# Performance work log

Measured on AMD Instinct MI355X. Metric: run time of the kernel, lower is better.

Reference implementation:

```python
import jax, jax.numpy as jnp
import numpy as np

N, E = 32768, 524288
NIN = NOUT = 64
EIN = 32
H, C = 4, 64
HC = H * C


def seg_softmax(logits, seg, num):
    m = jax.ops.segment_max(logits, seg, num_segments=num)
    m = jnp.where(jnp.isfinite(m), m, 0.0)
    ex = jnp.exp(logits - m[seg])
    s = jax.ops.segment_sum(ex, seg, num_segments=num)
    return ex / (s[seg] + 1e-16)


def setup_inputs() -> dict:
    key = jax.random.key(0)
    ks = iter(jax.random.split(key, 48))
    rn = lambda shape, s=0.05: jax.random.normal(next(ks), shape, jnp.float32) * s
    z = lambda shape: jnp.zeros(shape, jnp.float32)
    d = dict(
        x=rn((N, NIN), 1.0),
        edge_attr=rn((E, EIN), 1.0),
        # GINEConv 1: nn = mlp1 (64 -> 64 -> 64), edge lin (32 -> 64), eps
        eps1=z(()), w1a=rn((NIN, 64)), b1a=z((64,)), w1b=rn((64, NOUT)), b1b=z((NOUT,)),
        we1=rn((EIN, NIN)), be1=z((NIN,)),
        # GINEConv 2: nn = mlp2 (64 -> 32 -> 64), edge lin (32 -> 64), eps
        eps2=z(()), w2a=rn((NOUT, 32)), b2a=z((32,)), w2b=rn((32, NOUT)), b2b=z((NOUT,)),
        we2=rn((EIN, NOUT)), be2=z((NOUT,)),
        # TransformerConv(64, 64, heads=4, edge_dim=32)
        wq=rn((NOUT, HC)), bq=z((HC,)), wk=rn((NOUT, HC)), bk=z((HC,)),
        wv=rn((NOUT, HC)), bv=z((HC,)), we3=rn((EIN, HC)),
        wskip=rn((NOUT, HC)), bskip=z((HC,)),
        # GATv2Conv(256, 64, heads=1, edge_dim=32)
        wl=rn((HC, NOUT)), bl=z((NOUT,)), wr=rn((HC, NOUT)), br=z((NOUT,)),
        we4=rn((EIN, NOUT)), att=rn((NOUT,)), bias4=z((NOUT,)),
    )
    d['edge_index'] = jax.random.randint(next(ks), (2, E), 0, N, dtype=jnp.int64)
    return d


def _forward(x, edge_attr, eps1, w1a, b1a, w1b, b1b, we1, be1,
             eps2, w2a, b2a, w2b, b2b, we2, be2,
             wq, bq, wk, bk, wv, bv, we3, wskip, bskip,
             wl, bl, wr, br, we4, att, bias4, edge_index):
    src, dst = edge_index[0], edge_index[1]
    n = x.shape[0]

    # --- GINEConv 1: nn((1+eps)*x + sum_j relu(x_j + lin_e(e_ij))) ---
    e1 = edge_attr @ we1 + be1                                  # (E, NIN)
    agg = jax.ops.segment_sum(jax.nn.relu(x[src] + e1), dst, num_segments=n)
    h = (1.0 + eps1) * x + agg
    x = jax.nn.relu(h @ w1a + b1a) @ w1b + b1b                  # (N, NOUT)

    # --- GINEConv 2 ---
    e2 = edge_attr @ we2 + be2
    agg = jax.ops.segment_sum(jax.nn.relu(x[src] + e2), dst, num_segments=n)
    h = (1.0 + eps2) * x + agg
    x = jax.nn.relu(h @ w2a + b2a) @ w2b + b2b                  # (N, NOUT)

    # --- TransformerConv (heads=4, concat, root skip) ---
    q = (x @ wq + bq).reshape(n, H, C)
    k = (x @ wk + bk).reshape(n, H, C)
    v = (x @ wv + bv).reshape(n, H, C)
    e3 = (edge_attr @ we3).reshape(-1, H, C)
    kj = k[src] + e3
    alpha = jnp.einsum('ehc,ehc->eh', q[dst], kj) / jnp.sqrt(jnp.float32(C))
    alpha = seg_softmax(alpha, dst, n)                          # (E, H)
    msg = (v[src] + e3) * alpha[:, :, None]                     # (E, H, C)
    out = jax.ops.segment_sum(msg, dst, num_segments=n).reshape(n, HC)
    x = out + x @ wskip + bskip                                 # (N, 256)

    # --- GATv2Conv (heads=1) ---
    xl = x @ wl + bl                                            # (N, NOUT)
    xr = x @ wr + br
    e4 = edge_attr @ we4
    hmsg = jax.nn.leaky_relu(xl[src] + xr[dst] + e4, 0.2)       # (E, NOUT)
    logit = hmsg @ att                                          # (E,)
    a = seg_softmax(logit, dst, n)
    x = jax.ops.segment_sum(xl[src] * a[:, None], dst, num_segments=n) + bias4
    return x


def reference(x, edge_attr, eps1, w1a, b1a, w1b, b1b, we1, be1,
              eps2, w2a, b2a, w2b, b2b, we2, be2,
              wq, bq, wk, bk, wv, bv, we3, wskip, bskip,
              wl, bl, wr, br, we4, att, bias4, edge_index):
    return _forward(x, edge_attr, eps1, w1a, b1a, w1b, b1b, we1, be1,
                    eps2, w2a, b2a, w2b, b2b, we2, be2,
                    wq, bq, wk, bk, wv, bv, we3, wskip, bskip,
                    wl, bl, wr, br, we4, att, bias4, edge_index)
```

## Files before the change

kernel.cpp:

```cpp
#include <hip/hip_runtime.h>
#include <math.h>


typedef __attribute__((ext_vector_type(2))) _Float16 half2v;
typedef __attribute__((ext_vector_type(4))) _Float16 half4v;
typedef __attribute__((ext_vector_type(8))) _Float16 half8v;
typedef __attribute__((ext_vector_type(4))) float float4v;

__global__ void k_detect(const unsigned int* __restrict__ w, int* __restrict__ flag)
{
    __shared__ int any;
    if (threadIdx.x == 0) any = 0;
    __syncthreads();
    int found = 0;
    for (int i = threadIdx.x; i < 2048; i += 256)
        if (w[2 * i + 1] != 0u) found = 1;
    if (found) atomicOr(&any, 1);
    __syncthreads();
    if (threadIdx.x == 0) flag[0] = any ? 0 : 1;
}

__global__ void k_cvt(const void* __restrict__ eidx, const int* __restrict__ flag,
                      int* __restrict__ out, int* __restrict__ counts, int E)
{
    int i = blockIdx.x * blockDim.x + threadIdx.x;
    if (i >= 2 * E) return;
    int v = flag[0] ? (int)((const long long*)eidx)[i] : ((const int*)eidx)[i];
    out[i] = v;
    if (i >= E) atomicAdd(&counts[v], 1);
}

__global__ void k_scan(const int* __restrict__ counts, int* __restrict__ offs,
                       int* __restrict__ cursor, int N)
{
    __shared__ int part[1024];
    int t = threadIdx.x;
    int base = t * 32;
    int loc[32];
    int s = 0;
#pragma unroll
    for (int i = 0; i < 32; i++) { loc[i] = counts[base + i]; s += loc[i]; }
    part[t] = s;
    __syncthreads();
    for (int off = 1; off < 1024; off <<= 1) {
        int v = (t >= off) ? part[t - off] : 0;
        __syncthreads();
        part[t] += v;
        __syncthreads();
    }
    int run = part[t] - s;
#pragma unroll
    for (int i = 0; i < 32; i++) {
        offs[base + i] = run;
        cursor[base + i] = run;
        run += loc[i];
    }
    if (t == 1023) offs[N] = run;
}

__global__ void k_scatter(const int* __restrict__ dst, const int* __restrict__ srcA,
                          int* __restrict__ cursor, int* __restrict__ perm,
                          int* __restrict__ sperm, int E)
{
    int i = blockIdx.x * blockDim.x + threadIdx.x;
    if (i >= E) return;
    int d = dst[i];
    int p = atomicAdd(&cursor[d], 1);
    perm[p] = i;
    sperm[p] = srcA[i];
}

template<int WEAP, int DUAL>
__global__ __launch_bounds__(256) void k_emm2(
    const float* __restrict__ ea, const int* __restrict__ perm,
    const _Float16* __restrict__ WtA, const float* __restrict__ beA,
    _Float16* __restrict__ epA,
    const _Float16* __restrict__ WtB, const float* __restrict__ beB,
    _Float16* __restrict__ epB,
    _Float16* __restrict__ eap)
{
    __shared__ _Float16 st[4][16][72];
    int t = threadIdx.x;
    int wid = t >> 6, l = t & 63;
    int jb = (blockIdx.x * 4 + wid) * 16;
    int cr = l & 15, kg = l >> 4;
    int e = perm[jb + cr];
    const float* ar = ea + (size_t)e * 32 + kg * 8;
    float4 f0 = *(const float4*)ar;
    float4 f1 = *(const float4*)(ar + 4);
    half8v a;
    a[0] = (_Float16)f0.x; a[1] = (_Float16)f0.y;
    a[2] = (_Float16)f0.z; a[3] = (_Float16)f0.w;
    a[4] = (_Float16)f1.x; a[5] = (_Float16)f1.y;
    a[6] = (_Float16)f1.z; a[7] = (_Float16)f1.w;
    if (WEAP)
        *(half8v*)&eap[(size_t)(jb + cr) * 32 + kg * 8] = a;
    _Float16 (*S)[72] = st[wid];
    int rr = l >> 2, cs = (l & 3) * 16;
#pragma unroll
    for (int c = 0; c < 4; c++) {
        half8v b = *(const half8v*)&WtA[(size_t)(c * 16 + cr) * 32 + kg * 8];
        float4v d = __builtin_amdgcn_mfma_f32_16x16x32_f16(a, b, (float4v){0.f,0.f,0.f,0.f}, 0, 0, 0);
        int col = c * 16 + cr;
        float bv = beA ? beA[col] : 0.f;
#pragma unroll
        for (int r = 0; r < 4; r++)
            S[kg * 4 + r][col] = (_Float16)(d[r] + bv);
    }
    {
        half8v v0 = *(const half8v*)&S[rr][cs];
        half8v v1 = *(const half8v*)&S[rr][cs + 8];
        *(half8v*)&epA[(size_t)(jb + rr) * 64 + cs] = v0;
        *(half8v*)&epA[(size_t)(jb + rr) * 64 + cs + 8] = v1;
    }
    if (DUAL) {
#pragma unroll
        for (int c = 0; c < 4; c++) {
            half8v b = *(const half8v*)&WtB[(size_t)(c * 16 + cr) * 32 + kg * 8];
            float4v d = __builtin_amdgcn_mfma_f32_16x16x32_f16(a, b, (float4v){0.f,0.f,0.f,0.f}, 0, 0, 0);
            int col = c * 16 + cr;
            float bv = beB ? beB[col] : 0.f;
#pragma unroll
            for (int r = 0; r < 4; r++)
                S[kg * 4 + r][col] = (_Float16)(d[r] + bv);
        }
        half8v v0 = *(const half8v*)&S[rr][cs];
        half8v v1 = *(const half8v*)&S[rr][cs + 8];
        *(half8v*)&epB[(size_t)(jb + rr) * 64 + cs] = v0;
        *(half8v*)&epB[(size_t)(jb + rr) * 64 + cs + 8] = v1;
    }
}

__global__ __launch_bounds__(256) void k_emm(
    const _Float16* __restrict__ eap,
    const _Float16* __restrict__ WtA, const float* __restrict__ beA,
    _Float16* __restrict__ epA)
{
    __shared__ _Float16 st[4][16][72];
    int t = threadIdx.x;
    int wid = t >> 6, l = t & 63;
    int jb = (blockIdx.x * 4 + wid) * 16;
    int cr = l & 15, kg = l >> 4;
    half8v a = *(const half8v*)&eap[(size_t)(jb + cr) * 32 + kg * 8];
    _Float16 (*S)[72] = st[wid];
#pragma unroll
    for (int c = 0; c < 4; c++) {
        half8v b = *(const half8v*)&WtA[(size_t)(c * 16 + cr) * 32 + kg * 8];
        float4v d = __builtin_amdgcn_mfma_f32_16x16x32_f16(a, b, (float4v){0.f,0.f,0.f,0.f}, 0, 0, 0);
        int col = c * 16 + cr;
        float bv = beA ? beA[col] : 0.f;
#pragma unroll
        for (int r = 0; r < 4; r++)
            S[kg * 4 + r][col] = (_Float16)(d[r] + bv);
    }
    int rr = l >> 2, cs = (l & 3) * 16;
    half8v v0 = *(const half8v*)&S[rr][cs];
    half8v v1 = *(const half8v*)&S[rr][cs + 8];
    *(half8v*)&epA[(size_t)(jb + rr) * 64 + cs] = v0;
    *(half8v*)&epA[(size_t)(jb + rr) * 64 + cs + 8] = v1;
}

__global__ __launch_bounds__(256) void k_prep(
    const float* __restrict__ x, int NX,
    const float* __restrict__ wq, const float* __restrict__ wk,
    const float* __restrict__ wv, const float* __restrict__ wskip,
    const float* __restrict__ wl, const float* __restrict__ wr,
    const float* __restrict__ w1a, const float* __restrict__ w1b,
    const float* __restrict__ w2a, const float* __restrict__ w2b,
    const float* __restrict__ we3, const float* __restrict__ bq,
    const float* __restrict__ we1, const float* __restrict__ we2,
    const float* __restrict__ we4,
    _Float16* __restrict__ xh,
    _Float16* __restrict__ Wts, _Float16* __restrict__ Gt,
    _Float16* __restrict__ Wtl, _Float16* __restrict__ Wtr,
    _Float16* __restrict__ Wt1a, _Float16* __restrict__ Wt1b,
    _Float16* __restrict__ Wt2a, _Float16* __restrict__ Wt2b,
    _Float16* __restrict__ Mt, float* __restrict__ cst,
    _Float16* __restrict__ Wt1e, _Float16* __restrict__ Wt2e,
    _Float16* __restrict__ Wt4e, float* __restrict__ zt,
    _Float16* __restrict__ Bt3)
{
    int g = blockIdx.x * 256 + threadIdx.x;
    if (g < 16384) {
        int c = g >> 6, k = g & 63;
        Wts[g] = (_Float16)wskip[(size_t)k * 256 + c];
    } else if (g < 32768) {
        int q = g - 16384, col = q >> 6, d = q & 63;
        int h = col >> 6, c = col & 63;
        float s = 0.f;
        for (int mq = 0; mq < 64; mq++)
            s = fmaf(wq[(size_t)d * 256 + h * 64 + mq],
                     wk[(size_t)c * 256 + h * 64 + mq], s);
        Gt[q] = (_Float16)(0.125f * s);
    } else if (g < 49152) {
        int q = g - 32768, c = q >> 8, k = q & 255;
        Wtl[q] = (_Float16)wl[(size_t)k * 64 + c];
        Wtr[q] = (_Float16)wr[(size_t)k * 64 + c];
    } else if (g < 53248) {
        int q = g - 49152, m = q >> 6, k = q & 63;
        Wt1a[q] = (_Float16)w1a[(size_t)k * 64 + m];
        Wt1b[q] = (_Float16)w1b[(size_t)k * 64 + m];
    } else if (g < 55296) {
        int q = g - 53248, m = q >> 6, k = q & 63;
        Wt2a[q] = (_Float16)w2a[(size_t)k * 32 + m];
    } else if (g < 57344) {
        int q = g - 55296, c = q >> 5, k = q & 31;
        Wt2b[q] = (_Float16)w2b[(size_t)k * 64 + c];
    } else if (g < 65536) {
        int q = g - 57344, m = q >> 6, d = q & 63;
        int h = m >> 5, kk = m & 31;
        float s = 0.f;
        for (int c = 0; c < 64; c++)
            s = fmaf(wq[(size_t)d * 256 + h * 64 + c],
                     we3[(size_t)kk * 256 + h * 64 + c], s);
        Mt[q] = (_Float16)(0.125f * s);
    } else if (g < 65664) {
        int m = g - 65536, h = m >> 5, kk = m & 31;
        float s = 0.f;
        for (int c = 0; c < 64; c++)
            s = fmaf(bq[h * 64 + c], we3[(size_t)kk * 256 + h * 64 + c], s);
        cst[m] = 0.125f * s;
    } else if (g < 67712) {
        int q = g - 65664, c = q >> 5, k = q & 31;
        Wt1e[q] = (_Float16)we1[(size_t)k * 64 + c];
    } else if (g < 69760) {
        int q = g - 67712, c = q >> 5, k = q & 31;
        Wt2e[q] = (_Float16)we2[(size_t)k * 64 + c];
    } else if (g < 71808) {
        int q = g - 69760, c = q >> 5, k = q & 31;
        Wt4e[q] = (_Float16)we4[(size_t)k * 64 + c];
    } else if (g < 72064) {
        int q = g - 71808, h = q >> 6, c = q & 63;
        float s = 0.f;
        for (int mq = 0; mq < 64; mq++)
            s = fmaf(wk[(size_t)c * 256 + h * 64 + mq], bq[h * 64 + mq], s);
        zt[q] = 0.125f * s;
    } else if (g < 96640) {
        int q = g - 72064;
        int hc = q / 96, k = q - hc * 96;
        int h = hc >> 6, col = hc & 63;
        float v = (k < 64) ? wv[(size_t)k * 256 + h * 64 + col]
                           : we3[(size_t)(k - 64) * 256 + h * 64 + col];
        Bt3[q] = (_Float16)v;
    }
    for (int i = g; i < NX; i += 512 * 256)
        xh[i] = (_Float16)x[i];
}

template<int MID>
__global__ __launch_bounds__(256) void k_mlp(
    const _Float16* __restrict__ A,
    const _Float16* __restrict__ Wt1, const float* __restrict__ b1,
    const _Float16* __restrict__ Wt2, const float* __restrict__ b2,
    _Float16* __restrict__ out)
{
    __shared__ _Float16 As[64][72];
    __shared__ _Float16 Ws1[MID][72];
    __shared__ _Float16 Ws2[64][MID + 8];
    __shared__ _Float16 mids[64][MID + 8];
    int t = threadIdx.x;
    int n0 = blockIdx.x * 64;
    for (int f = t; f < 512; f += 256) {
        int r = f >> 3, seg = f & 7;
        *(uint4*)&As[r][seg * 8] = *(const uint4*)&A[(size_t)(n0 + r) * 64 + seg * 8];
    }
    for (int f = t; f < MID * 8; f += 256) {
        int r = f >> 3, seg = f & 7;
        *(uint4*)&Ws1[r][seg * 8] = *(const uint4*)&Wt1[(size_t)r * 64 + seg * 8];
    }
    constexpr int CH = MID / 8;
    for (int f = t; f < 64 * CH; f += 256) {
        int r = f / CH, seg = f % CH;
        *(uint4*)&Ws2[r][seg * 8] = *(const uint4*)&Wt2[(size_t)r * MID + seg * 8];
    }
    __syncthreads();
    int w = t >> 6, l = t & 63;
    int arow = w * 16 + (l & 15);
    int kg = (l >> 4) * 8;
    int colg = l & 15;
    int orow = w * 16 + (l >> 4) * 4;
    half8v a0 = *(const half8v*)&As[arow][kg];
    half8v a1 = *(const half8v*)&As[arow][32 + kg];
    constexpr int NCT1 = MID / 16;
#pragma unroll
    for (int ct = 0; ct < NCT1; ct++) {
        half8v b0 = *(const half8v*)&Ws1[ct * 16 + colg][kg];
        half8v b1v = *(const half8v*)&Ws1[ct * 16 + colg][32 + kg];
        float4v acc = {0.f, 0.f, 0.f, 0.f};
        acc = __builtin_amdgcn_mfma_f32_16x16x32_f16(a0, b0, acc, 0, 0, 0);
        acc = __builtin_amdgcn_mfma_f32_16x16x32_f16(a1, b1v, acc, 0, 0, 0);
        int col = ct * 16 + colg;
        float bb = b1[col];
#pragma unroll
        for (int r = 0; r < 4; r++)
            mids[orow + r][col] = (_Float16)fmaxf(acc[r] + bb, 0.f);
    }
    __syncthreads();
    half8v m0 = *(const half8v*)&mids[arow][kg];
#pragma unroll
    for (int ct = 0; ct < 4; ct++) {
        half8v b0 = *(const half8v*)&Ws2[ct * 16 + colg][kg];
        float4v acc = {0.f, 0.f, 0.f, 0.f};
        acc = __builtin_amdgcn_mfma_f32_16x16x32_f16(m0, b0, acc, 0, 0, 0);
        if (MID == 64) {
            half8v m1 = *(const half8v*)&mids[arow][32 + kg];
            half8v b1v = *(const half8v*)&Ws2[ct * 16 + colg][32 + kg];
            acc = __builtin_amdgcn_mfma_f32_16x16x32_f16(m1, b1v, acc, 0, 0, 0);
        }
        int col = ct * 16 + colg;
        float bb = b2[col];
#pragma unroll
        for (int r = 0; r < 4; r++)
            out[(size_t)(n0 + orow + r) * 64 + col] = (_Float16)(acc[r] + bb);
    }
}

__global__ __launch_bounds__(256) void k_gemm4m(
    const _Float16* __restrict__ A,
    const _Float16* __restrict__ Gt,
    const _Float16* __restrict__ Wts, const float* __restrict__ bs,
    const _Float16* __restrict__ Mt,  const float* __restrict__ cst,
    _Float16* __restrict__ Yb, _Float16* __restrict__ skiph,
    _Float16* __restrict__ qtp)
{
    __shared__ _Float16 As[64][72];
    __shared__ _Float16 Ws[128][72];
    int t = threadIdx.x;
    int n0 = blockIdx.x * 64;
    int y = blockIdx.y;
    for (int f = t; f < 512; f += 256) {
        int r = f >> 3, seg = f & 7;
        *(uint4*)&As[r][seg * 8] = *(const uint4*)&A[(size_t)(n0 + r) * 64 + seg * 8];
    }
    if (y < 8) {
        int j0 = (y & 3) * 64;
        const _Float16* Wt = (y < 4) ? Gt : Wts;
        for (int f = t; f < 512; f += 256) {
            int c = f >> 3, seg = f & 7;
            *(uint4*)&Ws[c][seg * 8] = *(const uint4*)&Wt[(size_t)(j0 + c) * 64 + seg * 8];
        }
    } else {
        for (int f = t; f < 1024; f += 256) {
            int c = f >> 3, seg = f & 7;
            *(uint4*)&Ws[c][seg * 8] = *(const uint4*)&Mt[(size_t)c * 64 + seg * 8];
        }
    }
    __syncthreads();
    int w = t >> 6, l = t & 63;
    int arow = w * 16 + (l & 15);
    int kg = (l >> 4) * 8;
    int colg = l & 15;
    int orow = w * 16 + (l >> 4) * 4;
    half8v a0 = *(const half8v*)&As[arow][kg];
    half8v a1 = *(const half8v*)&As[arow][32 + kg];
    if (y < 8) {
        int j0 = (y & 3) * 64;
        _Float16* O = (y < 4) ? Yb : skiph;
#pragma unroll
        for (int ct = 0; ct < 4; ct++) {
            half8v b0 = *(const half8v*)&Ws[ct * 16 + colg][kg];
            half8v b1 = *(const half8v*)&Ws[ct * 16 + colg][32 + kg];
            float4v a = {0.f, 0.f, 0.f, 0.f};
            a = __builtin_amdgcn_mfma_f32_16x16x32_f16(a0, b0, a, 0, 0, 0);
            a = __builtin_amdgcn_mfma_f32_16x16x32_f16(a1, b1, a, 0, 0, 0);
            int col = j0 + ct * 16 + colg;
            float bb = (y < 4) ? 0.f : bs[col];
#pragma unroll
            for (int r = 0; r < 4; r++)
                O[(size_t)(n0 + orow + r) * 256 + col] = (_Float16)(a[r] + bb);
        }
    } else {
#pragma unroll
        for (int ct = 0; ct < 8; ct++) {
            half8v b0 = *(const half8v*)&Ws[ct * 16 + colg][kg];
            half8v b1 = *(const half8v*)&Ws[ct * 16 + colg][32 + kg];
            float4v a = {0.f, 0.f, 0.f, 0.f};
            a = __builtin_amdgcn_mfma_f32_16x16x32_f16(a0, b0, a, 0, 0, 0);
            a = __builtin_amdgcn_mfma_f32_16x16x32_f16(a1, b1, a, 0, 0, 0);
            int col = ct * 16 + colg;
            float bb = cst[col];
#pragma unroll
            for (int r = 0; r < 4; r++)
                qtp[(size_t)(n0 + orow + r) * 128 + col] = (_Float16)(a[r] + bb);
        }
    }
}

__global__ __launch_bounds__(256) void k_gine2(
    const _Float16* __restrict__ xin, const _Float16* __restrict__ ep,
    const float* __restrict__ epsp,
    const int* __restrict__ offs, const int* __restrict__ sperm,
    _Float16* __restrict__ hout)
{
    int t = threadIdx.x;
    int wid  = __builtin_amdgcn_readfirstlane(t >> 6);
    int n    = blockIdx.x * 4 + wid;
    int lane = t & 63;
    int g = lane >> 4, li = lane & 15, c0 = li * 4;
    int j0 = __builtin_amdgcn_readfirstlane(offs[n]);
    int j1 = __builtin_amdgcn_readfirstlane(offs[n + 1]);
    float4 acc = {0.f, 0.f, 0.f, 0.f};
    for (int jq = j0; jq < j1; jq += 4) {
        int j = jq + g;
        int jc = (j < j1) ? j : (j1 - 1);
        int s = sperm[jc];
        half4v ev = *(const half4v*)&ep[(size_t)jc * 64 + c0];
        half4v xv = *(const half4v*)&xin[(size_t)s * 64 + c0];
        if (j < j1) {
            acc.x += fmaxf((float)xv[0] + (float)ev[0], 0.f);
            acc.y += fmaxf((float)xv[1] + (float)ev[1], 0.f);
            acc.z += fmaxf((float)xv[2] + (float)ev[2], 0.f);
            acc.w += fmaxf((float)xv[3] + (float)ev[3], 0.f);
        }
    }
    acc.x += __shfl_xor(acc.x, 16); acc.x += __shfl_xor(acc.x, 32);
    acc.y += __shfl_xor(acc.y, 16); acc.y += __shfl_xor(acc.y, 32);
    acc.z += __shfl_xor(acc.z, 16); acc.z += __shfl_xor(acc.z, 32);
    acc.w += __shfl_xor(acc.w, 16); acc.w += __shfl_xor(acc.w, 32);
    if (g == 0) {
        float eps1 = 1.f + epsp[0];
        half4v xn = *(const half4v*)&xin[(size_t)n * 64 + c0];
        half4v o;
        o[0] = (_Float16)(eps1 * (float)xn[0] + acc.x);
        o[1] = (_Float16)(eps1 * (float)xn[1] + acc.y);
        o[2] = (_Float16)(eps1 * (float)xn[2] + acc.z);
        o[3] = (_Float16)(eps1 * (float)xn[3] + acc.w);
        *(half4v*)&hout[(size_t)n * 64 + c0] = o;
    }
}

template<int USE_EAP>
__global__ __launch_bounds__(256) void k_tconv5(
    const _Float16* __restrict__ Yb, const _Float16* __restrict__ qtp,
    const float* __restrict__ zt, const _Float16* __restrict__ x2h,
    const _Float16* __restrict__ eap, const float* __restrict__ ea,
    const int* __restrict__ perm, const int* __restrict__ offs,
    const int* __restrict__ sperm,
    _Float16* __restrict__ xaccb, _Float16* __restrict__ wab,
    float* __restrict__ lb)
{
    int t = threadIdx.x;
    int wid = __builtin_amdgcn_readfirstlane(t >> 6);
    int n = blockIdx.x * 4 + wid;
    int lane = t & 63;
    int h = lane >> 4, c = lane & 15;
    float yb0, yb1, yb2, yb3;
    {
        half4v Y4 = *(const half4v*)&Yb[(size_t)n * 256 + h * 64 + c * 4];
        float4 z4 = *(const float4*)&zt[h * 64 + c * 4];
        yb0 = (float)Y4[0] + z4.x; yb1 = (float)Y4[1] + z4.y;
        yb2 = (float)Y4[2] + z4.z; yb3 = (float)Y4[3] + z4.w;
    }
    half2v qt2 = *(const half2v*)&qtp[(size_t)n * 128 + h * 32 + c * 2];
    float qt0 = (float)qt2[0], qt1 = (float)qt2[1];
    int j0 = __builtin_amdgcn_readfirstlane(offs[n]);
    int j1 = __builtin_amdgcn_readfirstlane(offs[n + 1]);
    float l = 0.f;
    float xa0 = 0.f, xa1 = 0.f, xa2 = 0.f, xa3 = 0.f;
    float wa0 = 0.f, wa1 = 0.f;
    int j = j0;
    for (; j + 1 < j1; j += 2) {
        int s0 = __builtin_amdgcn_readfirstlane(sperm[j]);
        int s1 = __builtin_amdgcn_readfirstlane(sperm[j + 1]);
        half4v xA = *(const half4v*)&x2h[(size_t)s0 * 64 + c * 4];
        half4v xB = *(const half4v*)&x2h[(size_t)s1 * 64 + c * 4];
        float eA0, eA1, eB0, eB1;
        if (USE_EAP) {
            half2v vA = *(const half2v*)&eap[(size_t)j * 32 + c * 2];
            half2v vB = *(const half2v*)&eap[(size_t)(j + 1) * 32 + c * 2];
            eA0 = (float)vA[0]; eA1 = (float)vA[1];
            eB0 = (float)vB[0]; eB1 = (float)vB[1];
        } else {
            int e0 = __builtin_amdgcn_readfirstlane(perm[j]);
            int e1 = __builtin_amdgcn_readfirstlane(perm[j + 1]);
            float2 fA = *(const float2*)&ea[(size_t)e0 * 32 + c * 2];
            float2 fB = *(const float2*)&ea[(size_t)e1 * 32 + c * 2];
            eA0 = fA.x; eA1 = fA.y; eB0 = fB.x; eB1 = fB.y;
        }
        float xA0 = (float)xA[0], xA1f = (float)xA[1];
        float xA2 = (float)xA[2], xA3 = (float)xA[3];
        float xB0 = (float)xB[0], xB1f = (float)xB[1];
        float xB2 = (float)xB[2], xB3 = (float)xB[3];
        float p0 = yb0 * xA0 + yb1 * xA1f + yb2 * xA2 + yb3 * xA3
                 + qt0 * eA0 + qt1 * eA1;
        float p1 = yb0 * xB0 + yb1 * xB1f + yb2 * xB2 + yb3 * xB3
                 + qt0 * eB0 + qt1 * eB1;
        p0 += __shfl_xor(p0, 1); p1 += __shfl_xor(p1, 1);
        p0 += __shfl_xor(p0, 2); p1 += __shfl_xor(p1, 2);
        p0 += __shfl_xor(p0, 4); p1 += __shfl_xor(p1, 4);
        p0 += __shfl_xor(p0, 8); p1 += __shfl_xor(p1, 8);
        float w0 = __expf(p0), w1 = __expf(p1);
        l += w0 + w1;
        xa0 += w0 * xA0 + w1 * xB0;
        xa1 += w0 * xA1f + w1 * xB1f;
        xa2 += w0 * xA2 + w1 * xB2;
        xa3 += w0 * xA3 + w1 * xB3;
        wa0 += w0 * eA0 + w1 * eB0;
        wa1 += w0 * eA1 + w1 * eB1;
    }
    if (j < j1) {
        int s0 = __builtin_amdgcn_readfirstlane(sperm[j]);
        half4v xA = *(const half4v*)&x2h[(size_t)s0 * 64 + c * 4];
        float eA0, eA1;
        if (USE_EAP) {
            half2v vA = *(const half2v*)&eap[(size_t)j * 32 + c * 2];
            eA0 = (float)vA[0]; eA1 = (float)vA[1];
        } else {
            int e0 = __builtin_amdgcn_readfirstlane(perm[j]);
            float2 fA = *(const float2*)&ea[(size_t)e0 * 32 + c * 2];
            eA0 = fA.x; eA1 = fA.y;
        }
        float xA0 = (float)xA[0], xA1f = (float)xA[1];
        float xA2 = (float)xA[2], xA3 = (float)xA[3];
        float p0 = yb0 * xA0 + yb1 * xA1f + yb2 * xA2 + yb3 * xA3
                 + qt0 * eA0 + qt1 * eA1;
        p0 += __shfl_xor(p0, 1); p0 += __shfl_xor(p0, 2);
        p0 += __shfl_xor(p0, 4); p0 += __shfl_xor(p0, 8);
        float w0 = __expf(p0);
        l += w0;
        xa0 += w0 * xA0; xa1 += w0 * xA1f; xa2 += w0 * xA2; xa3 += w0 * xA3;
        wa0 += w0 * eA0; wa1 += w0 * eA1;
    }
    half4v xo;
    xo[0] = (_Float16)xa0; xo[1] = (_Float16)xa1;
    xo[2] = (_Float16)xa2; xo[3] = (_Float16)xa3;
    *(half4v*)&xaccb[(size_t)n * 256 + h * 64 + c * 4] = xo;
    half2v wo;
    wo[0] = (_Float16)wa0; wo[1] = (_Float16)wa1;
    *(half2v*)&wab[(size_t)n * 128 + h * 32 + c * 2] = wo;
    if (c == 0) lb[n * 4 + h] = l;
}

__global__ __launch_bounds__(256) void k_tpost(
    const _Float16* __restrict__ xaccb, const _Float16* __restrict__ wab,
    const float* __restrict__ lb, const _Float16* __restrict__ Bt3,
    const float* __restrict__ bv, _Float16* __restrict__ skiph)
{
    int t = threadIdx.x;
    int h = t >> 6;
    int l = t & 63;
    int n0 = blockIdx.x * 64;
    int colg = l & 15, kg = (l >> 4) * 8;
    half8v Bf[4][3];
#pragma unroll
    for (int ct = 0; ct < 4; ct++) {
        size_t cb = (size_t)(h * 64 + ct * 16 + colg) * 96;
        Bf[ct][0] = *(const half8v*)&Bt3[cb + kg];
        Bf[ct][1] = *(const half8v*)&Bt3[cb + 32 + kg];
        Bf[ct][2] = *(const half8v*)&Bt3[cb + 64 + kg];
    }
#pragma unroll
    for (int rt = 0; rt < 4; rt++) {
        int arow = n0 + rt * 16 + (l & 15);
        half8v A0 = *(const half8v*)&xaccb[(size_t)arow * 256 + h * 64 + kg];
        half8v A1 = *(const half8v*)&xaccb[(size_t)arow * 256 + h * 64 + 32 + kg];
        half8v A2 = *(const half8v*)&wab[(size_t)arow * 128 + h * 32 + kg];
#pragma unroll
        for (int ct = 0; ct < 4; ct++) {
            float4v acc = {0.f, 0.f, 0.f, 0.f};
            acc = __builtin_amdgcn_mfma_f32_16x16x32_f16(A0, Bf[ct][0], acc, 0, 0, 0);
            acc = __builtin_amdgcn_mfma_f32_16x16x32_f16(A1, Bf[ct][1], acc, 0, 0, 0);
            acc = __builtin_amdgcn_mfma_f32_16x16x32_f16(A2, Bf[ct][2], acc, 0, 0, 0);
            int col = h * 64 + ct * 16 + colg;
            float bvc = bv[col];
#pragma unroll
            for (int r = 0; r < 4; r++) {
                int row = n0 + rt * 16 + (l >> 4) * 4 + r;
                float lv = lb[row * 4 + h];
                float rl = (lv > 0.f) ? 1.f / lv : 0.f;
                float bterm = (lv > 0.f) ? bvc : 0.f;
                size_t o = (size_t)row * 256 + col;
                float out = acc[r] * rl + bterm + (float)skiph[o];
                skiph[o] = (_Float16)out;
            }
        }
    }
}

__global__ __launch_bounds__(256) void k_gatgemm(
    const _Float16* __restrict__ A,
    const _Float16* __restrict__ WtL, const float* __restrict__ bL,
    const _Float16* __restrict__ WtR, const float* __restrict__ bR,
    _Float16* __restrict__ xlh, _Float16* __restrict__ xrh)
{
    __shared__ _Float16 As[64][136];
    __shared__ _Float16 WsL[64][136];
    __shared__ _Float16 WsR[64][136];
    int t = threadIdx.x;
    int n0 = blockIdx.x * 64;
    int w = t >> 6, l = t & 63;
    int arow = w * 16 + (l & 15);
    int kg = (l >> 4) * 8;
    int colg = l & 15;
    int orow = w * 16 + (l >> 4) * 4;
    float4v accL[4] = {{0.f,0.f,0.f,0.f},{0.f,0.f,0.f,0.f},
                       {0.f,0.f,0.f,0.f},{0.f,0.f,0.f,0.f}};
    float4v accR[4] = {{0.f,0.f,0.f,0.f},{0.f,0.f,0.f,0.f},
                       {0.f,0.f,0.f,0.f},{0.f,0.f,0.f,0.f}};
    for (int kh = 0; kh < 2; kh++) {
        __syncthreads();
        for (int f = t; f < 1024; f += 256) {
            int r = f >> 4, seg = f & 15;
            *(uint4*)&As[r][seg * 8] =
                *(const uint4*)&A[(size_t)(n0 + r) * 256 + kh * 128 + seg * 8];
            *(uint4*)&WsL[r][seg * 8] =
                *(const uint4*)&WtL[(size_t)r * 256 + kh * 128 + seg * 8];
            *(uint4*)&WsR[r][seg * 8] =
                *(const uint4*)&WtR[(size_t)r * 256 + kh * 128 + seg * 8];
        }
        __syncthreads();
#pragma unroll
        for (int ks = 0; ks < 4; ks++) {
            half8v a = *(const half8v*)&As[arow][ks * 32 + kg];
#pragma unroll
            for (int ct = 0; ct < 4; ct++) {
                half8v bl_ = *(const half8v*)&WsL[ct * 16 + colg][ks * 32 + kg];
                half8v br_ = *(const half8v*)&WsR[ct * 16 + colg][ks * 32 + kg];
                accL[ct] = __builtin_amdgcn_mfma_f32_16x16x32_f16(a, bl_, accL[ct], 0, 0, 0);
                accR[ct] = __builtin_amdgcn_mfma_f32_16x16x32_f16(a, br_, accR[ct], 0, 0, 0);
            }
        }
    }
#pragma unroll
    for (int ct = 0; ct < 4; ct++) {
        int col = ct * 16 + colg;
        float bvL = bL[col], bvR = bR[col];
#pragma unroll
        for (int r = 0; r < 4; r++) {
            xlh[(size_t)(n0 + orow + r) * 64 + col] = (_Float16)(accL[ct][r] + bvL);
            xrh[(size_t)(n0 + orow + r) * 64 + col] = (_Float16)(accR[ct][r] + bvR);
        }
    }
}

__global__ __launch_bounds__(256) void k_gat2(
    const _Float16* __restrict__ xl, const _Float16* __restrict__ xr,
    const _Float16* __restrict__ e4p,
    const float* __restrict__ attv, const float* __restrict__ bias4,
    const int* __restrict__ offs, const int* __restrict__ sperm,
    float* __restrict__ out)
{
    int t = threadIdx.x;
    int wid  = __builtin_amdgcn_readfirstlane(t >> 6);
    int n    = blockIdx.x * 4 + wid;
    int lane = t & 63;
    int g = lane >> 4, li = lane & 15, c0 = li * 4;
    half4v xrh = *(const half4v*)&xr[(size_t)n * 64 + c0];
    float xr0 = (float)xrh[0], xr1 = (float)xrh[1];
    float xr2 = (float)xrh[2], xr3 = (float)xrh[3];
    float4 av  = *(const float4*)&attv[c0];
    int j0 = __builtin_amdgcn_readfirstlane(offs[n]);
    int j1 = __builtin_amdgcn_readfirstlane(offs[n + 1]);
    float l = 0.f;
    float4 acc = {0.f, 0.f, 0.f, 0.f};
    for (int jq = j0; jq < j1; jq += 4) {
        int j = jq + g;
        int jc = (j < j1) ? j : (j1 - 1);
        int s = sperm[jc];
        half4v ev = *(const half4v*)&e4p[(size_t)jc * 64 + c0];
        half4v xlv = *(const half4v*)&xl[(size_t)s * 64 + c0];
        float x0 = (float)xlv[0], x1 = (float)xlv[1];
        float x2 = (float)xlv[2], x3 = (float)xlv[3];
        float h0 = x0 + xr0 + (float)ev[0];
        float h1 = x1 + xr1 + (float)ev[1];
        float h2 = x2 + xr2 + (float)ev[2];
        float h3 = x3 + xr3 + (float)ev[3];
        h0 = (h0 > 0.f) ? h0 : 0.2f * h0;
        h1 = (h1 > 0.f) ? h1 : 0.2f * h1;
        h2 = (h2 > 0.f) ? h2 : 0.2f * h2;
        h3 = (h3 > 0.f) ? h3 : 0.2f * h3;
        float p = h0 * av.x + h1 * av.y + h2 * av.z + h3 * av.w;
        p += __shfl_xor(p, 1); p += __shfl_xor(p, 2);
        p += __shfl_xor(p, 4); p += __shfl_xor(p, 8);
        float w = (j < j1) ? __expf(p) : 0.f;
        l += w;
        acc.x = fmaf(w, x0, acc.x);
        acc.y = fmaf(w, x1, acc.y);
        acc.z = fmaf(w, x2, acc.z);
        acc.w = fmaf(w, x3, acc.w);
    }
    l += __shfl_xor(l, 16); l += __shfl_xor(l, 32);
    acc.x += __shfl_xor(acc.x, 16); acc.x += __shfl_xor(acc.x, 32);
    acc.y += __shfl_xor(acc.y, 16); acc.y += __shfl_xor(acc.y, 32);
    acc.z += __shfl_xor(acc.z, 16); acc.z += __shfl_xor(acc.z, 32);
    acc.w += __shfl_xor(acc.w, 16); acc.w += __shfl_xor(acc.w, 32);
    if (g == 0) {
        float rl = 1.f / (l + 1e-16f);
        float4 bv = *(const float4*)&bias4[c0];
        float4 o;
        o.x = acc.x * rl + bv.x;
        o.y = acc.y * rl + bv.y;
        o.z = acc.z * rl + bv.z;
        o.w = acc.w * rl + bv.w;
        *(float4*)&out[(size_t)n * 64 + c0] = o;
    }
}

extern "C" void kernel_launch(void* const* d_in, const int* in_sizes, int n_in,
                              void* d_out, int out_size, void* d_ws, size_t ws_size,
                              hipStream_t stream)
{
    const float* x     = (const float*)d_in[0];
    const float* ea    = (const float*)d_in[1];
    const float* eps1  = (const float*)d_in[2];
    const float* w1a   = (const float*)d_in[3];
    const float* b1a   = (const float*)d_in[4];
    const float* w1b   = (const float*)d_in[5];
    const float* b1b   = (const float*)d_in[6];
    const float* we1   = (const float*)d_in[7];
    const float* be1   = (const float*)d_in[8];
    const float* eps2  = (const float*)d_in[9];
    const float* w2a   = (const float*)d_in[10];
    const float* b2a   = (const float*)d_in[11];
    const float* w2b   = (const float*)d_in[12];
    const float* b2b   = (const float*)d_in[13];
    const float* we2   = (const float*)d_in[14];
    const float* be2   = (const float*)d_in[15];
    const float* wq    = (const float*)d_in[16];
    const float* bq    = (const float*)d_in[17];
    const float* wk    = (const float*)d_in[18];
    const float* bk    = (const float*)d_in[19];
    const float* wv    = (const float*)d_in[20];
    const float* bvv   = (const float*)d_in[21];
    const float* we3   = (const float*)d_in[22];
    const float* wskip = (const float*)d_in[23];
    const float* bskip = (const float*)d_in[24];
    const float* wl    = (const float*)d_in[25];
    const float* bl    = (const float*)d_in[26];
    const float* wr    = (const float*)d_in[27];
    const float* br    = (const float*)d_in[28];
    const float* we4   = (const float*)d_in[29];
    const float* attv  = (const float*)d_in[30];
    const float* bias4 = (const float*)d_in[31];
    const void*  eidx  = d_in[32];
    (void)bk;

    const int N = in_sizes[0] / 64;
    const int E = in_sizes[1] / 32;

    char* ws = (char*)d_ws;
    size_t off = 0;
    auto alloc = [&](size_t bytes) {
        void* p = ws + off;
        off += (bytes + 255) & ~(size_t)255;
        return p;
    };
    int* flag    = (int*)alloc(4);
    int* econv   = (int*)alloc((size_t)2 * E * 4);
    int* counts  = (int*)alloc((size_t)N * 4);
    int* cursor  = (int*)alloc((size_t)N * 4);
    int* offs    = (int*)alloc((size_t)(N + 1) * 4);
    int* perm    = (int*)alloc((size_t)E * 4);
    int* sperm   = (int*)alloc((size_t)E * 4);
    _Float16* xh  = (_Float16*)alloc((size_t)N * 64 * 2);
    _Float16* h16 = (_Float16*)alloc((size_t)N * 64 * 2);
    _Float16* x1h = (_Float16*)alloc((size_t)N * 64 * 2);
    _Float16* x2h = (_Float16*)alloc((size_t)N * 64 * 2);
    _Float16* Wts  = (_Float16*)alloc(16384 * 2);
    _Float16* Gt   = (_Float16*)alloc(16384 * 2);
    _Float16* Wtl  = (_Float16*)alloc(16384 * 2);
    _Float16* Wtr  = (_Float16*)alloc(16384 * 2);
    _Float16* Wt1a = (_Float16*)alloc(4096 * 2);
    _Float16* Wt1b = (_Float16*)alloc(4096 * 2);
    _Float16* Wt2a = (_Float16*)alloc(2048 * 2);
    _Float16* Wt2b = (_Float16*)alloc(2048 * 2);
    _Float16* Mt   = (_Float16*)alloc(8192 * 2);
    float*    cst  = (float*)alloc(128 * 4);
    _Float16* Wt1e = (_Float16*)alloc(2048 * 2);
    _Float16* Wt2e = (_Float16*)alloc(2048 * 2);
    _Float16* Wt4e = (_Float16*)alloc(2048 * 2);
    float*    zt   = (float*)alloc(256 * 4);
    _Float16* Bt3  = (_Float16*)alloc(24576 * 2);
    char* R = (char*)alloc((size_t)2 * E * 64 * 2);
    _Float16* e1p = (_Float16*)R;
    _Float16* e2p = e1p + (size_t)E * 64;
    _Float16* Yb    = (_Float16*)R;
    _Float16* skiph = Yb + (size_t)N * 256;
    _Float16* qtp   = skiph + (size_t)N * 256;
    _Float16* xaccb = qtp + (size_t)N * 128;
    _Float16* wab   = xaccb + (size_t)N * 256;
    float*    lb    = (float*)(wab + (size_t)N * 128);
    _Float16* e4p = (_Float16*)R;
    _Float16* xlh = h16;
    _Float16* xrh = x1h;
    size_t base_off = off;
    _Float16* eap = (_Float16*)alloc((size_t)E * 32 * 2);
    int use_eap = (off <= ws_size) ? 1 : 0;

    if (base_off > ws_size) return;

    k_prep<<<512, 256, 0, stream>>>(x, N * 64, wq, wk, wv, wskip, wl, wr,
                                    w1a, w1b, w2a, w2b, we3, bq, we1, we2, we4,
                                    xh, Wts, Gt, Wtl, Wtr,
                                    Wt1a, Wt1b, Wt2a, Wt2b, Mt, cst,
                                    Wt1e, Wt2e, Wt4e, zt, Bt3);

    k_detect<<<1, 256, 0, stream>>>((const unsigned int*)eidx, flag);
    hipMemsetAsync(counts, 0, (size_t)N * 4, stream);
    k_cvt<<<(2 * E + 255) / 256, 256, 0, stream>>>(eidx, flag, econv, counts, E);
    const int* srcI = econv;
    const int* dstI = econv + E;

    k_scan<<<1, 1024, 0, stream>>>(counts, offs, cursor, N);
    k_scatter<<<(E + 255) / 256, 256, 0, stream>>>(dstI, srcI, cursor, perm, sperm, E);

    if (use_eap)
        k_emm2<1, 1><<<E / 64, 256, 0, stream>>>(ea, perm, Wt1e, be1, e1p,
                                                 Wt2e, be2, e2p, eap);
    else
        k_emm2<0, 1><<<E / 64, 256, 0, stream>>>(ea, perm, Wt1e, be1, e1p,
                                                 Wt2e, be2, e2p, eap);

    k_gine2<<<N / 4, 256, 0, stream>>>(xh, e1p, eps1, offs, sperm, h16);
    k_mlp<64><<<N / 64, 256, 0, stream>>>(h16, Wt1a, b1a, Wt1b, b1b, x1h);

    k_gine2<<<N / 4, 256, 0, stream>>>(x1h, e2p, eps2, offs, sperm, h16);
    k_mlp<32><<<N / 64, 256, 0, stream>>>(h16, Wt2a, b2a, Wt2b, b2b, x2h);

    k_gemm4m<<<dim3(N / 64, 9), 256, 0, stream>>>(x2h, Gt, Wts, bskip, Mt, cst,
                                                  Yb, skiph, qtp);
    if (use_eap)
        k_tconv5<1><<<N / 4, 256, 0, stream>>>(Yb, qtp, zt, x2h, eap, ea, perm,
                                               offs, sperm, xaccb, wab, lb);
    else
        k_tconv5<0><<<N / 4, 256, 0, stream>>>(Yb, qtp, zt, x2h, eap, ea, perm,
                                               offs, sperm, xaccb, wab, lb);
    k_tpost<<<N / 64, 256, 0, stream>>>(xaccb, wab, lb, Bt3, bvv, skiph);

    k_gatgemm<<<N / 64, 256, 0, stream>>>(skiph, Wtl, bl, Wtr, br, xlh, xrh);
    if (use_eap)
        k_emm<<<E / 64, 256, 0, stream>>>(eap, Wt4e, (const float*)nullptr, e4p);
    else
        k_emm2<0, 0><<<E / 64, 256, 0, stream>>>(ea, perm, Wt4e,
                                                 (const float*)nullptr, e4p,
                                                 (const _Float16*)nullptr,
                                                 (const float*)nullptr,
                                                 (_Float16*)nullptr,
                                                 (_Float16*)nullptr);
    k_gat2<<<N / 4, 256, 0, stream>>>(xlh, xrh, e4p, attv, bias4, offs, sperm,
                                      (float*)d_out);
}
```

Before: 347.9 us.

## Fuse GAT edge projection into first edge GEMM and unroll gather loops by two

Computes the GATv2 edge projection (edge_attr @ we4) in the same edge-matmul kernel that produces the GINE edge features, writing it to a new dedicated workspace buffer when there is room, and skips the separate e4 kernel launch later. The GINE and GAT aggregation loops now process two groups of four edges per iteration so more gathers are in flight at once. The fusion saves one pass over the edge attributes and a launch, at the cost of extra workspace memory. The unrolling raises register pressure.

```diff
diff --git a/kernel.cpp b/kernel.cpp
--- a/kernel.cpp
+++ b/kernel.cpp
@@ -70,13 +70,14 @@
     sperm[p] = srcA[i];
 }
 
-template<int WEAP, int DUAL>
+template<int WEAP, int DUAL, int E4>
 __global__ __launch_bounds__(256) void k_emm2(
     const float* __restrict__ ea, const int* __restrict__ perm,
     const _Float16* __restrict__ WtA, const float* __restrict__ beA,
     _Float16* __restrict__ epA,
     const _Float16* __restrict__ WtB, const float* __restrict__ beB,
     _Float16* __restrict__ epB,
+    const _Float16* __restrict__ Wt4, _Float16* __restrict__ ep4,
     _Float16* __restrict__ eap)
 {
     __shared__ _Float16 st[4][16][72];
@@ -128,6 +129,21 @@
         half8v v1 = *(const half8v*)&S[rr][cs + 8];
         *(half8v*)&epB[(size_t)(jb + rr) * 64 + cs] = v0;
         *(half8v*)&epB[(size_t)(jb + rr) * 64 + cs + 8] = v1;
+    }
+    if (E4) {
+#pragma unroll
+        for (int c = 0; c < 4; c++) {
+            half8v b = *(const half8v*)&Wt4[(size_t)(c * 16 + cr) * 32 + kg * 8];
+            float4v d = __builtin_amdgcn_mfma_f32_16x16x32_f16(a, b, (float4v){0.f,0.f,0.f,0.f}, 0, 0, 0);
+            int col = c * 16 + cr;
+#pragma unroll
+            for (int r = 0; r < 4; r++)
+                S[kg * 4 + r][col] = (_Float16)d[r];
+        }
+        half8v v0 = *(const half8v*)&S[rr][cs];
+        half8v v1 = *(const half8v*)&S[rr][cs + 8];
+        *(half8v*)&ep4[(size_t)(jb + rr) * 64 + cs] = v0;
+        *(half8v*)&ep4[(size_t)(jb + rr) * 64 + cs + 8] = v1;
     }
 }
 
@@ -400,17 +416,39 @@
     int j0 = __builtin_amdgcn_readfirstlane(offs[n]);
     int j1 = __builtin_amdgcn_readfirstlane(offs[n + 1]);
     float4 acc = {0.f, 0.f, 0.f, 0.f};
-    for (int jq = j0; jq < j1; jq += 4) {
-        int j = jq + g;
-        int jc = (j < j1) ? j : (j1 - 1);
-        int s = sperm[jc];
-        half4v ev = *(const half4v*)&ep[(size_t)jc * 64 + c0];
-        half4v xv = *(const half4v*)&xin[(size_t)s * 64 + c0];
-        if (j < j1) {
-            acc.x += fmaxf((float)xv[0] + (float)ev[0], 0.f);
-            acc.y += fmaxf((float)xv[1] + (float)ev[1], 0.f);
-            acc.z += fmaxf((float)xv[2] + (float)ev[2], 0.f);
-            acc.w += fmaxf((float)xv[3] + (float)ev[3], 0.f);
+    int jq = j0;
+    for (; jq + 4 < j1; jq += 8) {
+        int jA = jq + g;
+        int jB = jq + 4 + g;
+        int jcB = (jB < j1) ? jB : (j1 - 1);
+        int sA = sperm[jA];
+        int sB = sperm[jcB];
+        half4v evA = *(const half4v*)&ep[(size_t)jA * 64 + c0];
+        half4v evB = *(const half4v*)&ep[(size_t)jcB * 64 + c0];
+        half4v xvA = *(const half4v*)&xin[(size_t)sA * 64 + c0];
+        half4v xvB = *(const half4v*)&xin[(size_t)sB * 64 + c0];
+        acc.x += fmaxf((float)xvA[0] + (float)evA[0], 0.f);
+        acc.y += fmaxf((float)xvA[1] + (float)evA[1], 0.f);
+        acc.z += fmaxf((float)xvA[2] + (float)evA[2], 0.f);
+        acc.w += fmaxf((float)xvA[3] + (float)evA[3], 0.f);
+        if (jB < j1) {
+            acc.x += fmaxf((float)xvB[0] + (float)evB[0], 0.f);
+            acc.y += fmaxf((float)xvB[1] + (float)evB[1], 0.f);
+            acc.z += fmaxf((float)xvB[2] + (float)evB[2], 0.f);
+            acc.w += fmaxf((float)xvB[3] + (float)evB[3], 0.f);
+        }
+    }
+    if (jq < j1) {
+        int jA = jq + g;
+        int jcA = (jA < j1) ? jA : (j1 - 1);
+        int sA = sperm[jcA];
+        half4v evA = *(const half4v*)&ep[(size_t)jcA * 64 + c0];
+        half4v xvA = *(const half4v*)&xin[(size_t)sA * 64 + c0];
+        if (jA < j1) {
+            acc.x += fmaxf((float)xvA[0] + (float)evA[0], 0.f);
+            acc.y += fmaxf((float)xvA[1] + (float)evA[1], 0.f);
+            acc.z += fmaxf((float)xvA[2] + (float)evA[2], 0.f);
+            acc.w += fmaxf((float)xvA[3] + (float)evA[3], 0.f);
         }
     }
     acc.x += __shfl_xor(acc.x, 16); acc.x += __shfl_xor(acc.x, 32);
@@ -653,31 +691,73 @@
     int j1 = __builtin_amdgcn_readfirstlane(offs[n + 1]);
     float l = 0.f;
     float4 acc = {0.f, 0.f, 0.f, 0.f};
-    for (int jq = j0; jq < j1; jq += 4) {
-        int j = jq + g;
-        int jc = (j < j1) ? j : (j1 - 1);
-        int s = sperm[jc];
-        half4v ev = *(const half4v*)&e4p[(size_t)jc * 64 + c0];
-        half4v xlv = *(const half4v*)&xl[(size_t)s * 64 + c0];
-        float x0 = (float)xlv[0], x1 = (float)xlv[1];
-        float x2 = (float)xlv[2], x3 = (float)xlv[3];
-        float h0 = x0 + xr0 + (float)ev[0];
-        float h1 = x1 + xr1 + (float)ev[1];
-        float h2 = x2 + xr2 + (float)ev[2];
-        float h3 = x3 + xr3 + (float)ev[3];
-        h0 = (h0 > 0.f) ? h0 : 0.2f * h0;
-        h1 = (h1 > 0.f) ? h1 : 0.2f * h1;
-        h2 = (h2 > 0.f) ? h2 : 0.2f * h2;
-        h3 = (h3 > 0.f) ? h3 : 0.2f * h3;
-        float p = h0 * av.x + h1 * av.y + h2 * av.z + h3 * av.w;
-        p += __shfl_xor(p, 1); p += __shfl_xor(p, 2);
-        p += __shfl_xor(p, 4); p += __shfl_xor(p, 8);
-        float w = (j < j1) ? __expf(p) : 0.f;
-        l += w;
-        acc.x = fmaf(w, x0, acc.x);
-        acc.y = fmaf(w, x1, acc.y);
-        acc.z = fmaf(w, x2, acc.z);
-        acc.w = fmaf(w, x3, acc.w);
+    int jq = j0;
+    for (; jq + 4 < j1; jq += 8) {
+        int jA = jq + g;
+        int jB = jq + 4 + g;
+        int jcB = (jB < j1) ? jB : (j1 - 1);
+        int sA = sperm[jA];
+        int sB = sperm[jcB];
+        half4v evA = *(const half4v*)&e4p[(size_t)jA * 64 + c0];
+        half4v evB = *(const half4v*)&e4p[(size_t)jcB * 64 + c0];
+        half4v xlA = *(const half4v*)&xl[(size_t)sA * 64 + c0];
+        half4v xlB = *(const half4v*)&xl[(size_t)sB * 64 + c0];
+        float a0 = (float)xlA[0], a1 = (float)xlA[1];
+        float a2 = (float)xlA[2], a3 = (float)xlA[3];
+        float b0 = (float)xlB[0], b1 = (float)xlB[1];
+        float b2 = (float)xlB[2], b3 = (float)xlB[3];
+        float hA0 = a0 + xr0 + (float)evA[0];
+        float hA1 = a1 + xr1 + (float)evA[1];
+        float hA2 = a2 + xr2 + (float)evA[2];
+        float hA3 = a3 + xr3 + (float)evA[3];
+        float hB0 = b0 + xr0 + (float)evB[0];
+        float hB1 = b1 + xr1 + (float)evB[1];
+        float hB2 = b2 + xr2 + (float)evB[2];
+        float hB3 = b3 + xr3 + (float)evB[3];
+        hA0 = (hA0 > 0.f) ? hA0 : 0.2f * hA0;
+        hA1 = (hA1 > 0.f) ? hA1 : 0.2f * hA1;
+        hA2 = (hA2 > 0.f) ? hA2 : 0.2f * hA2;
+        hA3 = (hA3 > 0.f) ? hA3 : 0.2f * hA3;
+        hB0 = (hB0 > 0.f) ? hB0 : 0.2f * hB0;
+        hB1 = (hB1 > 0.f) ? hB1 : 0.2f * hB1;
+        hB2 = (hB2 > 0.f) ? hB2 : 0.2f * hB2;
+        hB3 = (hB3 > 0.f) ? hB3 : 0.2f * hB3;
+        float pA = hA0 * av.x + hA1 * av.y + hA2 * av.z + hA3 * av.w;
+        float pB = hB0 * av.x + hB1 * av.y + hB2 * av.z + hB3 * av.w;
+        pA += __shfl_xor(pA, 1); pB += __shfl_xor(pB, 1);
+        pA += __shfl_xor(pA, 2); pB += __shfl_xor(pB, 2);
+        pA += __shfl_xor(pA, 4); pB += __shfl_xor(pB, 4);
+        pA += __shfl_xor(pA, 8); pB += __shfl_xor(pB, 8);
+        float wA = __expf(pA);
+        float wB = (jB < j1) ? __expf(pB) : 0.f;
+        l += wA + wB;
+        acc.x += wA * a0 + wB * b0;
+        acc.y += wA * a1 + wB * b1;
+        acc.z += wA * a2 + wB * b2;
+        acc.w += wA * a3 + wB * b3;
+    }
+    if (jq < j1) {
+        int jA = jq + g;
+        int jcA = (jA < j1) ? jA : (j1 - 1);
+        int sA = sperm[jcA];
+        half4v evA = *(const half4v*)&e4p[(size_t)jcA * 64 + c0];
+        half4v xlA = *(const half4v*)&xl[(size_t)sA * 64 + c0];
+        float a0 = (float)xlA[0], a1 = (float)xlA[1];
+        float a2 = (float)xlA[2], a3 = (float)xlA[3];
+        float hA0 = a0 + xr0 + (float)evA[0];
+        float hA1 = a1 + xr1 + (float)evA[1];
+        float hA2 = a2 + xr2 + (float)evA[2];
+        float hA3 = a3 + xr3 + (float)evA[3];
+        hA0 = (hA0 > 0.f) ? hA0 : 0.2f * hA0;
+        hA1 = (hA1 > 0.f) ? hA1 : 0.2f * hA1;
+        hA2 = (hA2 > 0.f) ? hA2 : 0.2f * hA2;
+        hA3 = (hA3 > 0.f) ? hA3 : 0.2f * hA3;
+        float pA = hA0 * av.x + hA1 * av.y + hA2 * av.z + hA3 * av.w;
+        pA += __shfl_xor(pA, 1); pA += __shfl_xor(pA, 2);
+        pA += __shfl_xor(pA, 4); pA += __shfl_xor(pA, 8);
+        float wA = (jA < j1) ? __expf(pA) : 0.f;
+        l += wA;
+        acc.x += wA * a0; acc.y += wA * a1; acc.z += wA * a2; acc.w += wA * a3;
     }
     l += __shfl_xor(l, 16); l += __shfl_xor(l, 32);
     acc.x += __shfl_xor(acc.x, 16); acc.x += __shfl_xor(acc.x, 32);
@@ -780,12 +860,15 @@
     _Float16* xaccb = qtp + (size_t)N * 128;
     _Float16* wab   = xaccb + (size_t)N * 256;
     float*    lb    = (float*)(wab + (size_t)N * 128);
-    _Float16* e4p = (_Float16*)R;
+    _Float16* e4pR = (_Float16*)R;
     _Float16* xlh = h16;
     _Float16* xrh = x1h;
     size_t base_off = off;
     _Float16* eap = (_Float16*)alloc((size_t)E * 32 * 2);
     int use_eap = (off <= ws_size) ? 1 : 0;
+    _Float16* e4pX = (_Float16*)alloc((size_t)E * 64 * 2);
+    int use_e4 = (off <= ws_size) ? 1 : 0;
+    _Float16* e4p = use_e4 ? e4pX : e4pR;
 
     if (base_off > ws_size) return;
 
@@ -804,12 +887,20 @@
     k_scan<<<1, 1024, 0, stream>>>(counts, offs, cursor, N);
     k_scatter<<<(E + 255) / 256, 256, 0, stream>>>(dstI, srcI, cursor, perm, sperm, E);
 
-    if (use_eap)
-        k_emm2<1, 1><<<E / 64, 256, 0, stream>>>(ea, perm, Wt1e, be1, e1p,
-                                                 Wt2e, be2, e2p, eap);
+    if (use_e4)
+        k_emm2<1, 1, 1><<<E / 64, 256, 0, stream>>>(ea, perm, Wt1e, be1, e1p,
+                                                    Wt2e, be2, e2p, Wt4e, e4pX, eap);
+    else if (use_eap)
+        k_emm2<1, 1, 0><<<E / 64, 256, 0, stream>>>(ea, perm, Wt1e, be1, e1p,
+                                                    Wt2e, be2, e2p,
+                                                    (const _Float16*)nullptr,
+                                                    (_Float16*)nullptr, eap);
     else
-        k_emm2<0, 1><<<E / 64, 256, 0, stream>>>(ea, perm, Wt1e, be1, e1p,
-                                                 Wt2e, be2, e2p, eap);
+        k_emm2<0, 1, 0><<<E / 64, 256, 0, stream>>>(ea, perm, Wt1e, be1, e1p,
+                                                    Wt2e, be2, e2p,
+                                                    (const _Float16*)nullptr,
+                                                    (_Float16*)nullptr,
+                                                    (_Float16*)nullptr);
 
     k_gine2<<<N / 4, 256, 0, stream>>>(xh, e1p, eps1, offs, sperm, h16);
     k_mlp<64><<<N / 64, 256, 0, stream>>>(h16, Wt1a, b1a, Wt1b, b1b, x1h);
@@ -828,15 +919,19 @@
     k_tpost<<<N / 64, 256, 0, stream>>>(xaccb, wab, lb, Bt3, bvv, skiph);
 
     k_gatgemm<<<N / 64, 256, 0, stream>>>(skiph, Wtl, bl, Wtr, br, xlh, xrh);
-    if (use_eap)
-        k_emm<<<E / 64, 256, 0, stream>>>(eap, Wt4e, (const float*)nullptr, e4p);
-    else
-        k_emm2<0, 0><<<E / 64, 256, 0, stream>>>(ea, perm, Wt4e,
-                                                 (const float*)nullptr, e4p,
-                                                 (const _Float16*)nullptr,
-                                                 (const float*)nullptr,
-                                                 (_Float16*)nullptr,
-                                                 (_Float16*)nullptr);
+    if (!use_e4) {
+        if (use_eap)
+            k_emm<<<E / 64, 256, 0, stream>>>(eap, Wt4e, (const float*)nullptr, e4pR);
+        else
+            k_emm2<0, 0, 0><<<E / 64, 256, 0, stream>>>(ea, perm, Wt4e,
+                                                        (const float*)nullptr, e4pR,
+                                                        (const _Float16*)nullptr,
+                                                        (const float*)nullptr,
+                                                        (_Float16*)nullptr,
+                                                        (const _Float16*)nullptr,
+                                                        (_Float16*)nullptr,
+                                                        (_Float16*)nullptr);
+    }
     k_gat2<<<N / 4, 256, 0, stream>>>(xlh, xrh, e4p, attv, bias4, offs, sperm,
                                       (float*)d_out);
 }
```

After: 353.2 us. Within noise of the previous version (+1.5%).
